# Performance work log

Measured on AMD Instinct MI355X. Metric: run time of the kernel, lower is better.

Reference implementation:

```python
import jax, jax.numpy as jnp
import numpy as np

N_NODES = 100000
N_EDGES = 1600000
IN_DIM = 128
HID = 128
OUT_DIM = 64
NLP_DIM = 786  # 768 + 11 + 4 + 3
N_LAYERS = 3
N_USERS = 4096
BN_EPS = 1e-5


def setup_inputs() -> dict:
    key = jax.random.key(0)
    ks = jax.random.split(key, 24)
    inp = {
        "x": jax.random.normal(ks[0], (N_NODES, IN_DIM), jnp.float32),
        "nlp_features": jax.random.normal(ks[1], (NLP_DIM,), jnp.float32),
        "edge_index": jax.random.randint(ks[2], (2, N_EDGES), 0, N_NODES),
        "user_indices": jax.random.randint(ks[3], (N_USERS,), 0, N_NODES),
        # input projection
        "W_in": jax.random.normal(ks[4], (IN_DIM, HID), jnp.float32) / np.sqrt(IN_DIM),
        "b_in": jnp.zeros((HID,), jnp.float32),
        # GCN layers (stacked)
        "W_gnn": jax.random.normal(ks[5], (N_LAYERS, HID, HID), jnp.float32) / np.sqrt(HID),
        "b_gnn": jnp.zeros((N_LAYERS, HID), jnp.float32),
        # batchnorm running stats / affine (eval mode)
        "bn_gamma": jnp.ones((N_LAYERS, HID), jnp.float32),
        "bn_beta": jnp.zeros((N_LAYERS, HID), jnp.float32),
        "bn_mean": 0.1 * jax.random.normal(ks[6], (N_LAYERS, HID), jnp.float32),
        "bn_var": 0.5 + jax.random.uniform(ks[7], (N_LAYERS, HID), jnp.float32),
        # node embedding projection
        "W_proj": jax.random.normal(ks[8], (HID, OUT_DIM), jnp.float32) / np.sqrt(HID),
        "b_proj": jnp.zeros((OUT_DIM,), jnp.float32),
        # predictor MLP
        "W1": jax.random.normal(ks[9], (OUT_DIM + NLP_DIM, 256), jnp.float32) / np.sqrt(OUT_DIM + NLP_DIM),
        "b1": jnp.zeros((256,), jnp.float32),
        "W2": jax.random.normal(ks[10], (256, 128), jnp.float32) / np.sqrt(256.0),
        "b2": jnp.zeros((128,), jnp.float32),
        "W3": jax.random.normal(ks[11], (128, 1), jnp.float32) / np.sqrt(128.0),
        "b3": jnp.zeros((1,), jnp.float32),
    }
    return inp


def reference(x, nlp_features, edge_index, user_indices,
              W_in, b_in, W_gnn, b_gnn, bn_gamma, bn_beta, bn_mean, bn_var,
              W_proj, b_proj, W1, b1, W2, b2, W3, b3):
    n = x.shape[0]
    src, dst = edge_index[0], edge_index[1]
    # GCN normalization with self-loops: deg = in-degree + 1
    deg = jax.ops.segment_sum(jnp.ones_like(src, dtype=x.dtype), dst, num_segments=n) + 1.0
    dinv = jax.lax.rsqrt(deg)                      # [N]
    enorm = dinv[src] * dinv[dst]                  # [E]

    h = jax.nn.relu(x @ W_in + b_in)               # [N, HID]
    for i in range(W_gnn.shape[0]):
        hw = h @ W_gnn[i]                          # [N, HID]
        agg = jax.ops.segment_sum(enorm[:, None] * hw[src], dst, num_segments=n)
        agg = agg + (dinv * dinv)[:, None] * hw + b_gnn[i]  # self-loop + bias
        # batchnorm (eval: running stats) + relu; dropout is identity in eval
        hn = (agg - bn_mean[i]) * jax.lax.rsqrt(bn_var[i] + BN_EPS) * bn_gamma[i] + bn_beta[i]
        h = jax.nn.relu(hn)

    emb = h @ W_proj + b_proj                      # [N, OUT_DIM]
    u = emb[user_indices]                          # [B, OUT_DIM]
    nlp = jnp.broadcast_to(nlp_features, (u.shape[0], nlp_features.shape[0]))
    z = jnp.concatenate([u, nlp], axis=1)          # [B, OUT_DIM+NLP_DIM]
    z = jax.nn.relu(z @ W1 + b1)
    z = jax.nn.relu(z @ W2 + b2)
    probs = jax.nn.sigmoid(z @ W3 + b3)
    return probs.squeeze(-1)
```

## Files before the change

kernel.cpp:

```cpp
#include <hip/hip_runtime.h>
#include <math.h>

typedef _Float16 half4 __attribute__((ext_vector_type(4)));


__global__ __launch_bounds__(256) void hist_k(const int* __restrict__ dst, int* __restrict__ cnt,
                                              int* __restrict__ rank, int E){
  int e = blockIdx.x*256 + threadIdx.x;
  if (e < E) rank[e] = atomicAdd(&cnt[dst[e]], 1);
}

__global__ __launch_bounds__(256) void blocksum_k(const int* __restrict__ cnt, int* __restrict__ bsum, int N){
  int i = blockIdx.x*256 + threadIdx.x;
  int v = (i < N) ? cnt[i] : 0;
  #pragma unroll
  for (int off = 32; off; off >>= 1) v += __shfl_down(v, off, 64);
  __shared__ int s[4];
  if ((threadIdx.x & 63) == 0) s[threadIdx.x >> 6] = v;
  __syncthreads();
  if (threadIdx.x == 0) bsum[blockIdx.x] = s[0] + s[1] + s[2] + s[3];
}

__global__ __launch_bounds__(512) void scan_small_k(const int* __restrict__ bsum, int* __restrict__ boff, int NB){
  __shared__ int s[512];
  int t = threadIdx.x;
  int v = (t < NB) ? bsum[t] : 0;
  s[t] = v; __syncthreads();
  for (int off = 1; off < 512; off <<= 1){
    int x = (t >= off) ? s[t-off] : 0;
    __syncthreads();
    s[t] += x;
    __syncthreads();
  }
  if (t < NB) boff[t] = s[t] - v;
}

__global__ __launch_bounds__(256) void scan_final_k(const int* __restrict__ cnt, const int* __restrict__ boff,
                                                    int* __restrict__ rowptr,
                                                    float* __restrict__ dinv, int N){
  __shared__ int s[256];
  int t = threadIdx.x;
  int i = blockIdx.x*256 + t;
  int v = (i < N) ? cnt[i] : 0;
  s[t] = v; __syncthreads();
  for (int off = 1; off < 256; off <<= 1){
    int x = (t >= off) ? s[t-off] : 0;
    __syncthreads();
    s[t] += x;
    __syncthreads();
  }
  int excl = s[t] - v + boff[blockIdx.x];
  if (i < N){
    rowptr[i] = excl;
    dinv[i]   = rsqrtf((float)v + 1.0f);
    if (i == N-1) rowptr[N] = excl + v;
  }
}

__global__ __launch_bounds__(256) void fill_k(const int* __restrict__ src, const int* __restrict__ dst,
                                              const int* __restrict__ rowptr, const int* __restrict__ rank,
                                              int* __restrict__ col, int E){
  int e = blockIdx.x*256 + threadIdx.x;
  if (e >= E) return;
  col[rowptr[dst[e]] + rank[e]] = src[e];
}


template<int ACT, int SCALED>
__global__ __launch_bounds__(256) void gemm128_k(const float* __restrict__ A, const float* __restrict__ B,
                                                 const float* __restrict__ bias, float* __restrict__ Cf,
                                                 _Float16* __restrict__ Ch, const float* __restrict__ dinv,
                                                 int M, int N, int K){
  __shared__ float As[16][132];
  __shared__ float Bs[16][132];
  const int tid = threadIdx.x;
  const int m0 = blockIdx.x * 128, n0 = blockIdx.y * 128;
  const int ty = tid >> 4, tx = tid & 15;
  const int sar = tid >> 1, sak = (tid & 1) * 8;
  const int sbk = tid >> 4, sbn = (tid & 15) * 8;
  int arow = m0 + sar; if (arow >= M) arow = M - 1;

  float acc[8][8];
  #pragma unroll
  for (int i = 0; i < 8; ++i)
    #pragma unroll
    for (int j = 0; j < 8; ++j) acc[i][j] = 0.f;

  float4 a0 = *(const float4*)&A[(size_t)arow*K + 0 + sak];
  float4 a1 = *(const float4*)&A[(size_t)arow*K + 0 + sak + 4];
  float4 b0 = *(const float4*)&B[(size_t)(0+sbk)*N + n0 + sbn];
  float4 b1 = *(const float4*)&B[(size_t)(0+sbk)*N + n0 + sbn + 4];

  for (int k0 = 0; k0 < K; k0 += 16){
    __syncthreads();
    As[sak+0][sar]=a0.x; As[sak+1][sar]=a0.y; As[sak+2][sar]=a0.z; As[sak+3][sar]=a0.w;
    As[sak+4][sar]=a1.x; As[sak+5][sar]=a1.y; As[sak+6][sar]=a1.z; As[sak+7][sar]=a1.w;
    *(float4*)&Bs[sbk][sbn]   = b0;
    *(float4*)&Bs[sbk][sbn+4] = b1;
    __syncthreads();
    if (k0 + 16 < K){
      a0 = *(const float4*)&A[(size_t)arow*K + (k0+16) + sak];
      a1 = *(const float4*)&A[(size_t)arow*K + (k0+16) + sak + 4];
      b0 = *(const float4*)&B[(size_t)(k0+16+sbk)*N + n0 + sbn];
      b1 = *(const float4*)&B[(size_t)(k0+16+sbk)*N + n0 + sbn + 4];
    }
    #pragma unroll
    for (int kk = 0; kk < 16; ++kk){
      const float4 av0 = *(const float4*)&As[kk][ty*4];
      const float4 av1 = *(const float4*)&As[kk][64 + ty*4];
      const float4 bv0 = *(const float4*)&Bs[kk][tx*4];
      const float4 bv1 = *(const float4*)&Bs[kk][64 + tx*4];
      const float a[8] = {av0.x,av0.y,av0.z,av0.w,av1.x,av1.y,av1.z,av1.w};
      const float b[8] = {bv0.x,bv0.y,bv0.z,bv0.w,bv1.x,bv1.y,bv1.z,bv1.w};
      #pragma unroll
      for (int i = 0; i < 8; ++i)
        #pragma unroll
        for (int j = 0; j < 8; ++j)
          acc[i][j] += a[i]*b[j];
    }
  }

  float bl[8] = {0,0,0,0,0,0,0,0};
  if (!SCALED && bias){
    const float4 x0 = *(const float4*)&bias[n0 + tx*4];
    const float4 x1 = *(const float4*)&bias[n0 + 64 + tx*4];
    bl[0]=x0.x; bl[1]=x0.y; bl[2]=x0.z; bl[3]=x0.w;
    bl[4]=x1.x; bl[5]=x1.y; bl[6]=x1.z; bl[7]=x1.w;
  }
  #pragma unroll
  for (int i = 0; i < 8; ++i){
    int r = m0 + (i>>2)*64 + ty*4 + (i&3);
    if (r < M){
      if (SCALED){
        float di = dinv[r];
        half4 h0, h1;
        h0[0]=(_Float16)(di*acc[i][0]); h0[1]=(_Float16)(di*acc[i][1]);
        h0[2]=(_Float16)(di*acc[i][2]); h0[3]=(_Float16)(di*acc[i][3]);
        h1[0]=(_Float16)(di*acc[i][4]); h1[1]=(_Float16)(di*acc[i][5]);
        h1[2]=(_Float16)(di*acc[i][6]); h1[3]=(_Float16)(di*acc[i][7]);
        *(half4*)&Ch[(size_t)r*N + n0 + tx*4]      = h0;
        *(half4*)&Ch[(size_t)r*N + n0 + 64 + tx*4] = h1;
      } else {
        float4 o0, o1;
        o0.x = acc[i][0]+bl[0]; o0.y = acc[i][1]+bl[1]; o0.z = acc[i][2]+bl[2]; o0.w = acc[i][3]+bl[3];
        o1.x = acc[i][4]+bl[4]; o1.y = acc[i][5]+bl[5]; o1.z = acc[i][6]+bl[6]; o1.w = acc[i][7]+bl[7];
        if (ACT == 1){
          o0.x=fmaxf(o0.x,0.f); o0.y=fmaxf(o0.y,0.f); o0.z=fmaxf(o0.z,0.f); o0.w=fmaxf(o0.w,0.f);
          o1.x=fmaxf(o1.x,0.f); o1.y=fmaxf(o1.y,0.f); o1.z=fmaxf(o1.z,0.f); o1.w=fmaxf(o1.w,0.f);
        }
        *(float4*)&Cf[(size_t)r*N + n0 + tx*4]      = o0;
        *(float4*)&Cf[(size_t)r*N + n0 + 64 + tx*4] = o1;
      }
    }
  }
}


template<int ACT>
__global__ __launch_bounds__(256) void gemm_k(const float* __restrict__ A, const float* __restrict__ B,
                                              const float* __restrict__ bias, float* __restrict__ C,
                                              int M, int N, int K){
  __shared__ float As[16][68];
  __shared__ float Bs[16][68];
  int tid = threadIdx.x;
  int m0 = blockIdx.x * 64, n0 = blockIdx.y * 64;
  int ty = tid >> 4, tx = tid & 15;
  int lm = tid >> 2, lkq = tid & 3;
  int lk = tid >> 4, ln4 = tid & 15;
  int arow = m0 + lm; if (arow >= M) arow = M - 1;

  float acc[4][4] = {{0.f}};

  for (int k0 = 0; k0 < K; k0 += 16){
    float4 av = *(const float4*)&A[(size_t)arow*K + k0 + lkq*4];
    float4 bv = *(const float4*)&B[(size_t)(k0+lk)*N + n0 + ln4*4];
    As[lkq*4+0][lm] = av.x; As[lkq*4+1][lm] = av.y; As[lkq*4+2][lm] = av.z; As[lkq*4+3][lm] = av.w;
    *(float4*)&Bs[lk][ln4*4] = bv;
    __syncthreads();
    #pragma unroll
    for (int kk = 0; kk < 16; ++kk){
      const float4 a = *(const float4*)&As[kk][ty*4];
      const float4 b = *(const float4*)&Bs[kk][tx*4];
      acc[0][0] += a.x*b.x; acc[0][1] += a.x*b.y; acc[0][2] += a.x*b.z; acc[0][3] += a.x*b.w;
      acc[1][0] += a.y*b.x; acc[1][1] += a.y*b.y; acc[1][2] += a.y*b.z; acc[1][3] += a.y*b.w;
      acc[2][0] += a.z*b.x; acc[2][1] += a.z*b.y; acc[2][2] += a.z*b.z; acc[2][3] += a.z*b.w;
      acc[3][0] += a.w*b.x; acc[3][1] += a.w*b.y; acc[3][2] += a.w*b.z; acc[3][3] += a.w*b.w;
    }
    __syncthreads();
  }

  float bv0 = 0.f, bv1 = 0.f, bv2 = 0.f, bv3 = 0.f;
  if (bias){
    const float4 b4 = *(const float4*)&bias[n0 + tx*4];
    bv0 = b4.x; bv1 = b4.y; bv2 = b4.z; bv3 = b4.w;
  }
  #pragma unroll
  for (int i = 0; i < 4; ++i){
    int r = m0 + ty*4 + i;
    if (r < M){
      float4 o;
      o.x = acc[i][0] + bv0; o.y = acc[i][1] + bv1; o.z = acc[i][2] + bv2; o.w = acc[i][3] + bv3;
      if (ACT == 1){ o.x = fmaxf(o.x,0.f); o.y = fmaxf(o.y,0.f); o.z = fmaxf(o.z,0.f); o.w = fmaxf(o.w,0.f); }
      *(float4*)&C[(size_t)r*N + n0 + tx*4] = o;
    }
  }
}


__global__ __launch_bounds__(256) void agg_k(const _Float16* __restrict__ hws, float* __restrict__ hout,
                                             const int* __restrict__ rowptr, const int* __restrict__ col,
                                             const float* __restrict__ dinv,
                                             const float* __restrict__ bgnn, const float* __restrict__ gamma,
                                             const float* __restrict__ beta, const float* __restrict__ mean,
                                             const float* __restrict__ var, int N){
  int n = (blockIdx.x * blockDim.x + threadIdx.x) >> 6;
  if (n >= N) return;
  int lane = threadIdx.x & 63;
  int half = lane >> 5;
  int sl   = lane & 31;
  int f    = sl * 4;
  int beg = rowptr[n], end = rowptr[n+1];

  float4 A0 = make_float4(0.f,0.f,0.f,0.f);
  float4 A1 = make_float4(0.f,0.f,0.f,0.f);
  float4 A2 = make_float4(0.f,0.f,0.f,0.f);
  float4 A3 = make_float4(0.f,0.f,0.f,0.f);

  int j = beg + half;
  for (; j + 6 < end; j += 8){
    int s0 = col[j], s1 = col[j+2], s2 = col[j+4], s3 = col[j+6];
    const half4 v0 = *(const half4*)&hws[(size_t)s0*128 + f];
    const half4 v1 = *(const half4*)&hws[(size_t)s1*128 + f];
    const half4 v2 = *(const half4*)&hws[(size_t)s2*128 + f];
    const half4 v3 = *(const half4*)&hws[(size_t)s3*128 + f];
    A0.x += (float)v0[0]; A0.y += (float)v0[1]; A0.z += (float)v0[2]; A0.w += (float)v0[3];
    A1.x += (float)v1[0]; A1.y += (float)v1[1]; A1.z += (float)v1[2]; A1.w += (float)v1[3];
    A2.x += (float)v2[0]; A2.y += (float)v2[1]; A2.z += (float)v2[2]; A2.w += (float)v2[3];
    A3.x += (float)v3[0]; A3.y += (float)v3[1]; A3.z += (float)v3[2]; A3.w += (float)v3[3];
  }
  for (; j < end; j += 2){
    int s0 = col[j];
    const half4 v0 = *(const half4*)&hws[(size_t)s0*128 + f];
    A0.x += (float)v0[0]; A0.y += (float)v0[1]; A0.z += (float)v0[2]; A0.w += (float)v0[3];
  }
  A0.x += A1.x + A2.x + A3.x;
  A0.y += A1.y + A2.y + A3.y;
  A0.z += A1.z + A2.z + A3.z;
  A0.w += A1.w + A2.w + A3.w;

  A0.x += __shfl_xor(A0.x, 32, 64);
  A0.y += __shfl_xor(A0.y, 32, 64);
  A0.z += __shfl_xor(A0.z, 32, 64);
  A0.w += __shfl_xor(A0.w, 32, 64);

  if (half == 0){
    float di = dinv[n];
    const half4 hv = *(const half4*)&hws[(size_t)n*128 + f];
    const float4 bg = *(const float4*)&bgnn[f];
    const float4 gm = *(const float4*)&gamma[f];
    const float4 bt = *(const float4*)&beta[f];
    const float4 mn = *(const float4*)&mean[f];
    const float4 vr = *(const float4*)&var[f];
    float4 o;
    o.x = (di*(A0.x + (float)hv[0]) + bg.x - mn.x) * (gm.x * rsqrtf(vr.x + 1e-5f)) + bt.x;
    o.y = (di*(A0.y + (float)hv[1]) + bg.y - mn.y) * (gm.y * rsqrtf(vr.y + 1e-5f)) + bt.y;
    o.z = (di*(A0.z + (float)hv[2]) + bg.z - mn.z) * (gm.z * rsqrtf(vr.z + 1e-5f)) + bt.z;
    o.w = (di*(A0.w + (float)hv[3]) + bg.w - mn.w) * (gm.w * rsqrtf(vr.w + 1e-5f)) + bt.w;
    o.x = fmaxf(o.x, 0.f); o.y = fmaxf(o.y, 0.f); o.z = fmaxf(o.z, 0.f); o.w = fmaxf(o.w, 0.f);
    *(float4*)&hout[(size_t)n*128 + f] = o;
  }
}


__global__ __launch_bounds__(256) void gather_k(const float* __restrict__ h, const int* __restrict__ uidx,
                                                float* __restrict__ uh, int B){
  int g = blockIdx.x*256 + threadIdx.x;
  if (g >= B*128) return;
  int i = g >> 7, f = g & 127;
  uh[g] = h[(size_t)uidx[i]*128 + f];
}

__global__ __launch_bounds__(256) void initc1_k(const float* __restrict__ b1, float* __restrict__ c1){
  c1[threadIdx.x] = b1[threadIdx.x];
}

__global__ __launch_bounds__(256) void c1acc_k(const float* __restrict__ nlp, const float* __restrict__ W1,
                                               float* __restrict__ c1, int NLP){
  int b = blockIdx.x;
  int c  = (b & 3) * 64 + (threadIdx.x & 63);
  int dq = threadIdx.x >> 6;
  int d0 = (b >> 2) * 99;
  float acc = 0.f;
  for (int d = d0 + dq; d < d0 + 99 && d < NLP; d += 4)
    acc += nlp[d] * W1[(size_t)(64 + d) * 256 + c];
  __shared__ float s[256];
  s[threadIdx.x] = acc; __syncthreads();
  if (dq == 0){
    float t = s[threadIdx.x] + s[threadIdx.x + 64] + s[threadIdx.x + 128] + s[threadIdx.x + 192];
    atomicAdd(&c1[c], t);
  }
}

__global__ __launch_bounds__(256) void head_k(const float* __restrict__ z2, const float* __restrict__ W3,
                                              const float* __restrict__ b3, float* __restrict__ out, int B){
  int gid = blockIdx.x * blockDim.x + threadIdx.x;
  int u = gid >> 6, l = gid & 63;
  if (u >= B) return;
  float v = z2[(size_t)u*128 + l] * W3[l] + z2[(size_t)u*128 + 64 + l] * W3[64 + l];
  #pragma unroll
  for (int off = 32; off; off >>= 1) v += __shfl_down(v, off, 64);
  if (l == 0) out[u] = 1.f / (1.f + expf(-(v + b3[0])));
}


static void launch_gemm(int act, const float* A, const float* Bm, const float* bias, float* C,
                        int M, int N, int K, hipStream_t s){
  dim3 g((M + 63) / 64, N / 64);
  if (act) hipLaunchKernelGGL((gemm_k<1>), g, dim3(256), 0, s, A, Bm, bias, C, M, N, K);
  else     hipLaunchKernelGGL((gemm_k<0>), g, dim3(256), 0, s, A, Bm, bias, C, M, N, K);
}

extern "C" void kernel_launch(void* const* d_in, const int* in_sizes, int n_in,
                              void* d_out, int out_size, void* d_ws, size_t ws_size,
                              hipStream_t stream){
  const float* x     = (const float*)d_in[0];
  const float* nlp   = (const float*)d_in[1];
  const int*   eidx  = (const int*)  d_in[2];
  const int*   uidx  = (const int*)  d_in[3];
  const float* W_in  = (const float*)d_in[4];
  const float* b_in  = (const float*)d_in[5];
  const float* W_gnn = (const float*)d_in[6];
  const float* b_gnn = (const float*)d_in[7];
  const float* gam   = (const float*)d_in[8];
  const float* bet   = (const float*)d_in[9];
  const float* mean  = (const float*)d_in[10];
  const float* var   = (const float*)d_in[11];
  const float* Wproj = (const float*)d_in[12];
  const float* bproj = (const float*)d_in[13];
  const float* W1    = (const float*)d_in[14];
  const float* b1    = (const float*)d_in[15];
  const float* W2    = (const float*)d_in[16];
  const float* b2    = (const float*)d_in[17];
  const float* W3    = (const float*)d_in[18];
  const float* b3    = (const float*)d_in[19];
  float* out = (float*)d_out;

  const int N   = in_sizes[0] / 128;
  const int E   = in_sizes[2] / 2;
  const int B   = in_sizes[3];
  const int NLP = in_sizes[1];
  const int HID = 128;

  char* p = (char*)d_ws;
  auto carve = [&](size_t bytes) -> void* {
    void* q = (void*)p;
    p += (bytes + 255) & ~(size_t)255;
    return q;
  };
  int*      cnt    = (int*)     carve((size_t)N * 4);
  int*      rowptr = (int*)     carve((size_t)(N + 1) * 4);
  int*      rank   = (int*)     carve((size_t)E * 4);
  int*      bsum   = (int*)     carve(512 * 4);
  int*      boff   = (int*)     carve(512 * 4);
  float*    dinv   = (float*)   carve((size_t)N * 4);
  int*      col    = (int*)     carve((size_t)E * 4);
  float*    h      = (float*)   carve((size_t)N * HID * 4);
  _Float16* hws    = (_Float16*)carve((size_t)N * HID * 2);
  float*    uh     = (float*)   carve((size_t)B * HID * 4);
  float*    embu   = (float*)   carve((size_t)B * 64 * 4);
  float*    z1     = (float*)   carve((size_t)B * 256 * 4);
  float*    z2     = (float*)   carve((size_t)B * 128 * 4);
  float*    c1     = (float*)   carve(256 * 4);

  const int* src = eidx;
  const int* dst = eidx + E;

  const int NB = (N + 255) / 256;

  hipMemsetAsync(cnt, 0, (size_t)N * 4, stream);
  hipLaunchKernelGGL(hist_k, dim3((E + 255) / 256), dim3(256), 0, stream, dst, cnt, rank, E);
  hipLaunchKernelGGL(blocksum_k, dim3(NB), dim3(256), 0, stream, cnt, bsum, N);
  hipLaunchKernelGGL(scan_small_k, dim3(1), dim3(512), 0, stream, bsum, boff, NB);
  hipLaunchKernelGGL(scan_final_k, dim3(NB), dim3(256), 0, stream, cnt, boff, rowptr, dinv, N);
  hipLaunchKernelGGL(fill_k, dim3((E + 255) / 256), dim3(256), 0, stream, src, dst, rowptr, rank, col, E);

  {
    dim3 g((N + 127) / 128, HID / 128);
    hipLaunchKernelGGL((gemm128_k<1,0>), g, dim3(256), 0, stream,
                       x, W_in, b_in, h, (_Float16*)nullptr, (const float*)nullptr, N, HID, 128);
  }

  for (int i = 0; i < 3; ++i){
    dim3 g((N + 127) / 128, HID / 128);
    hipLaunchKernelGGL((gemm128_k<0,1>), g, dim3(256), 0, stream,
                       h, W_gnn + (size_t)i * 128 * 128, (const float*)nullptr,
                       (float*)nullptr, hws, dinv, N, HID, 128);
    hipLaunchKernelGGL(agg_k, dim3((N * 64 + 255) / 256), dim3(256), 0, stream,
                       hws, h, rowptr, col, dinv,
                       b_gnn + i * 128, gam + i * 128, bet + i * 128, mean + i * 128, var + i * 128, N);
  }

  hipLaunchKernelGGL(gather_k, dim3((B * 128 + 255) / 256), dim3(256), 0, stream, h, uidx, uh, B);
  hipLaunchKernelGGL(initc1_k, dim3(1), dim3(256), 0, stream, b1, c1);
  hipLaunchKernelGGL(c1acc_k, dim3(32), dim3(256), 0, stream, nlp, W1, c1, NLP);

  launch_gemm(0, uh, Wproj, bproj, embu, B, 64, 128, stream);
  launch_gemm(1, embu, W1, c1, z1, B, 256, 64, stream);
  launch_gemm(1, z1, W2, b2, z2, B, 128, 256, stream);
  hipLaunchKernelGGL(head_k, dim3((B * 64 + 255) / 256), dim3(256), 0, stream, z2, W3, b3, out, B);
}
```

Before: 698.1 us.

## Use MFMA fp16 GEMMs with swizzled LDS and store hidden state in fp16

Replaces the fp32 SIMT 128x128 GEMM with an MFMA 16x16x32 fp16 kernel. Weights are pre-transposed and converted to fp16, and both operands are staged in LDS with an XOR swizzle. The hidden state h is now stored in fp16, which halves GEMM input and aggregation output traffic, and the aggregation accumulates neighbours in fp16 half4 vectors instead of fp32. This lowers memory and compute cost but risks precision loss from fp16 accumulation over neighbour sums. The 64KB of LDS per block may also limit occupancy.

```diff
diff --git a/kernel.cpp b/kernel.cpp
--- a/kernel.cpp
+++ b/kernel.cpp
@@ -1,7 +1,9 @@
 #include <hip/hip_runtime.h>
 #include <math.h>
 
-typedef _Float16 half4 __attribute__((ext_vector_type(4)));
+typedef _Float16 half8_t __attribute__((ext_vector_type(8)));
+typedef _Float16 half4_t __attribute__((ext_vector_type(4)));
+typedef float    f32x4_t __attribute__((ext_vector_type(4)));
 
 
 __global__ __launch_bounds__(256) void hist_k(const int* __restrict__ dst, int* __restrict__ cnt,
@@ -66,90 +68,116 @@
 }
 
 
-template<int ACT, int SCALED>
-__global__ __launch_bounds__(256) void gemm128_k(const float* __restrict__ A, const float* __restrict__ B,
-                                                 const float* __restrict__ bias, float* __restrict__ Cf,
-                                                 _Float16* __restrict__ Ch, const float* __restrict__ dinv,
-                                                 int M, int N, int K){
-  __shared__ float As[16][132];
-  __shared__ float Bs[16][132];
+__global__ __launch_bounds__(256) void prepw_k(const float* __restrict__ Win, const float* __restrict__ Wgnn,
+                                               _Float16* __restrict__ Bt){
+  int idx = blockIdx.x*256 + threadIdx.x;
+  int m = idx >> 14;
+  int r = idx & 16383;
+  int k = r >> 7, n = r & 127;
+  const float* W = (m == 0) ? Win : (Wgnn + (size_t)(m-1)*16384);
+  Bt[(size_t)m*16384 + n*128 + k] = (_Float16)W[k*128 + n];
+}
+
+
+template<int AF16, int EPI>
+__global__ __launch_bounds__(256) void mgemm_k(const void* __restrict__ Ap, const _Float16* __restrict__ Bt,
+                                               const float* __restrict__ bias, const float* __restrict__ dinv,
+                                               _Float16* __restrict__ C, int M){
+  __shared__ _Float16 As[128*128];
+  __shared__ _Float16 Bs[128*128];
   const int tid = threadIdx.x;
-  const int m0 = blockIdx.x * 128, n0 = blockIdx.y * 128;
-  const int ty = tid >> 4, tx = tid & 15;
-  const int sar = tid >> 1, sak = (tid & 1) * 8;
-  const int sbk = tid >> 4, sbn = (tid & 15) * 8;
-  int arow = m0 + sar; if (arow >= M) arow = M - 1;
-
-  float acc[8][8];
-  #pragma unroll
-  for (int i = 0; i < 8; ++i)
-    #pragma unroll
-    for (int j = 0; j < 8; ++j) acc[i][j] = 0.f;
-
-  float4 a0 = *(const float4*)&A[(size_t)arow*K + 0 + sak];
-  float4 a1 = *(const float4*)&A[(size_t)arow*K + 0 + sak + 4];
-  float4 b0 = *(const float4*)&B[(size_t)(0+sbk)*N + n0 + sbn];
-  float4 b1 = *(const float4*)&B[(size_t)(0+sbk)*N + n0 + sbn + 4];
-
-  for (int k0 = 0; k0 < K; k0 += 16){
-    __syncthreads();
-    As[sak+0][sar]=a0.x; As[sak+1][sar]=a0.y; As[sak+2][sar]=a0.z; As[sak+3][sar]=a0.w;
-    As[sak+4][sar]=a1.x; As[sak+5][sar]=a1.y; As[sak+6][sar]=a1.z; As[sak+7][sar]=a1.w;
-    *(float4*)&Bs[sbk][sbn]   = b0;
-    *(float4*)&Bs[sbk][sbn+4] = b1;
-    __syncthreads();
-    if (k0 + 16 < K){
-      a0 = *(const float4*)&A[(size_t)arow*K + (k0+16) + sak];
-      a1 = *(const float4*)&A[(size_t)arow*K + (k0+16) + sak + 4];
-      b0 = *(const float4*)&B[(size_t)(k0+16+sbk)*N + n0 + sbn];
-      b1 = *(const float4*)&B[(size_t)(k0+16+sbk)*N + n0 + sbn + 4];
-    }
-    #pragma unroll
-    for (int kk = 0; kk < 16; ++kk){
-      const float4 av0 = *(const float4*)&As[kk][ty*4];
-      const float4 av1 = *(const float4*)&As[kk][64 + ty*4];
-      const float4 bv0 = *(const float4*)&Bs[kk][tx*4];
-      const float4 bv1 = *(const float4*)&Bs[kk][64 + tx*4];
-      const float a[8] = {av0.x,av0.y,av0.z,av0.w,av1.x,av1.y,av1.z,av1.w};
-      const float b[8] = {bv0.x,bv0.y,bv0.z,bv0.w,bv1.x,bv1.y,bv1.z,bv1.w};
+  const int m0 = blockIdx.x * 128;
+
+  {
+    int n = tid >> 1, kb = (tid & 1) * 64;
+    const half8_t* srcb = (const half8_t*)(Bt + n*128 + kb);
+    #pragma unroll
+    for (int q = 0; q < 8; ++q){
+      uint32_t byte = (uint32_t)(n*256 + kb*2 + q*16) ^ (uint32_t)((n & 7) << 4);
+      *(half8_t*)((char*)Bs + byte) = srcb[q];
+    }
+  }
+  {
+    int rr = tid >> 1, kb = (tid & 1) * 64;
+    int row = m0 + rr; if (row >= M) row = M - 1;
+    if (AF16){
+      const half8_t* srca = (const half8_t*)((const _Float16*)Ap + (size_t)row*128 + kb);
       #pragma unroll
-      for (int i = 0; i < 8; ++i)
-        #pragma unroll
-        for (int j = 0; j < 8; ++j)
-          acc[i][j] += a[i]*b[j];
-    }
-  }
-
-  float bl[8] = {0,0,0,0,0,0,0,0};
-  if (!SCALED && bias){
-    const float4 x0 = *(const float4*)&bias[n0 + tx*4];
-    const float4 x1 = *(const float4*)&bias[n0 + 64 + tx*4];
-    bl[0]=x0.x; bl[1]=x0.y; bl[2]=x0.z; bl[3]=x0.w;
-    bl[4]=x1.x; bl[5]=x1.y; bl[6]=x1.z; bl[7]=x1.w;
-  }
-  #pragma unroll
-  for (int i = 0; i < 8; ++i){
-    int r = m0 + (i>>2)*64 + ty*4 + (i&3);
-    if (r < M){
-      if (SCALED){
-        float di = dinv[r];
-        half4 h0, h1;
-        h0[0]=(_Float16)(di*acc[i][0]); h0[1]=(_Float16)(di*acc[i][1]);
-        h0[2]=(_Float16)(di*acc[i][2]); h0[3]=(_Float16)(di*acc[i][3]);
-        h1[0]=(_Float16)(di*acc[i][4]); h1[1]=(_Float16)(di*acc[i][5]);
-        h1[2]=(_Float16)(di*acc[i][6]); h1[3]=(_Float16)(di*acc[i][7]);
-        *(half4*)&Ch[(size_t)r*N + n0 + tx*4]      = h0;
-        *(half4*)&Ch[(size_t)r*N + n0 + 64 + tx*4] = h1;
-      } else {
-        float4 o0, o1;
-        o0.x = acc[i][0]+bl[0]; o0.y = acc[i][1]+bl[1]; o0.z = acc[i][2]+bl[2]; o0.w = acc[i][3]+bl[3];
-        o1.x = acc[i][4]+bl[4]; o1.y = acc[i][5]+bl[5]; o1.z = acc[i][6]+bl[6]; o1.w = acc[i][7]+bl[7];
-        if (ACT == 1){
-          o0.x=fmaxf(o0.x,0.f); o0.y=fmaxf(o0.y,0.f); o0.z=fmaxf(o0.z,0.f); o0.w=fmaxf(o0.w,0.f);
-          o1.x=fmaxf(o1.x,0.f); o1.y=fmaxf(o1.y,0.f); o1.z=fmaxf(o1.z,0.f); o1.w=fmaxf(o1.w,0.f);
+      for (int q = 0; q < 8; ++q){
+        uint32_t byte = (uint32_t)(rr*256 + kb*2 + q*16) ^ (uint32_t)((rr & 7) << 4);
+        *(half8_t*)((char*)As + byte) = srca[q];
+      }
+    } else {
+      const float4* srca = (const float4*)((const float*)Ap + (size_t)row*128 + kb);
+      #pragma unroll
+      for (int q = 0; q < 8; ++q){
+        float4 f0 = srca[2*q], f1 = srca[2*q+1];
+        half8_t h;
+        h[0]=(_Float16)f0.x; h[1]=(_Float16)f0.y; h[2]=(_Float16)f0.z; h[3]=(_Float16)f0.w;
+        h[4]=(_Float16)f1.x; h[5]=(_Float16)f1.y; h[6]=(_Float16)f1.z; h[7]=(_Float16)f1.w;
+        uint32_t byte = (uint32_t)(rr*256 + kb*2 + q*16) ^ (uint32_t)((rr & 7) << 4);
+        *(half8_t*)((char*)As + byte) = h;
+      }
+    }
+  }
+  __syncthreads();
+
+  const int w = tid >> 6, lane = tid & 63;
+  const int l15 = lane & 15, lq = lane >> 4;
+
+  f32x4_t acc[2][8];
+  #pragma unroll
+  for (int rg = 0; rg < 2; ++rg)
+    #pragma unroll
+    for (int cg = 0; cg < 8; ++cg)
+      acc[rg][cg] = (f32x4_t){0.f,0.f,0.f,0.f};
+
+  #pragma unroll
+  for (int ks = 0; ks < 4; ++ks){
+    half8_t a[2], b[8];
+    #pragma unroll
+    for (int rg = 0; rg < 2; ++rg){
+      int row = w*32 + rg*16 + l15;
+      uint32_t byte = (uint32_t)(row*256 + (ks*32 + lq*8)*2) ^ (uint32_t)((row & 7) << 4);
+      a[rg] = *(const half8_t*)((const char*)As + byte);
+    }
+    #pragma unroll
+    for (int cg = 0; cg < 8; ++cg){
+      int coln = cg*16 + l15;
+      uint32_t byte = (uint32_t)(coln*256 + (ks*32 + lq*8)*2) ^ (uint32_t)((coln & 7) << 4);
+      b[cg] = *(const half8_t*)((const char*)Bs + byte);
+    }
+    #pragma unroll
+    for (int rg = 0; rg < 2; ++rg)
+      #pragma unroll
+      for (int cg = 0; cg < 8; ++cg)
+        acc[rg][cg] = __builtin_amdgcn_mfma_f32_16x16x32_f16(a[rg], b[cg], acc[rg][cg], 0, 0, 0);
+  }
+
+  float bl[8];
+  if (EPI == 0){
+    #pragma unroll
+    for (int cg = 0; cg < 8; ++cg) bl[cg] = bias[cg*16 + l15];
+  }
+
+  #pragma unroll
+  for (int rg = 0; rg < 2; ++rg){
+    #pragma unroll
+    for (int r = 0; r < 4; ++r){
+      int grow = m0 + w*32 + rg*16 + lq*4 + r;
+      if (grow < M){
+        if (EPI == 1){
+          float di = dinv[grow];
+          #pragma unroll
+          for (int cg = 0; cg < 8; ++cg)
+            C[(size_t)grow*128 + cg*16 + l15] = (_Float16)(di * acc[rg][cg][r]);
+        } else {
+          #pragma unroll
+          for (int cg = 0; cg < 8; ++cg){
+            float v = acc[rg][cg][r] + bl[cg];
+            C[(size_t)grow*128 + cg*16 + l15] = (_Float16)fmaxf(v, 0.f);
+          }
         }
-        *(float4*)&Cf[(size_t)r*N + n0 + tx*4]      = o0;
-        *(float4*)&Cf[(size_t)r*N + n0 + 64 + tx*4] = o1;
       }
     }
   }
@@ -207,7 +235,7 @@
 }
 
 
-__global__ __launch_bounds__(256) void agg_k(const _Float16* __restrict__ hws, float* __restrict__ hout,
+__global__ __launch_bounds__(256) void agg_k(const _Float16* __restrict__ hws, _Float16* __restrict__ hout,
                                              const int* __restrict__ rowptr, const int* __restrict__ col,
                                              const float* __restrict__ dinv,
                                              const float* __restrict__ bgnn, const float* __restrict__ gamma,
@@ -221,32 +249,26 @@
   int f    = sl * 4;
   int beg = rowptr[n], end = rowptr[n+1];
 
-  float4 A0 = make_float4(0.f,0.f,0.f,0.f);
-  float4 A1 = make_float4(0.f,0.f,0.f,0.f);
-  float4 A2 = make_float4(0.f,0.f,0.f,0.f);
-  float4 A3 = make_float4(0.f,0.f,0.f,0.f);
+  half4_t H0 = {0,0,0,0}, H1 = {0,0,0,0}, H2 = {0,0,0,0}, H3 = {0,0,0,0};
 
   int j = beg + half;
   for (; j + 6 < end; j += 8){
     int s0 = col[j], s1 = col[j+2], s2 = col[j+4], s3 = col[j+6];
-    const half4 v0 = *(const half4*)&hws[(size_t)s0*128 + f];
-    const half4 v1 = *(const half4*)&hws[(size_t)s1*128 + f];
-    const half4 v2 = *(const half4*)&hws[(size_t)s2*128 + f];
-    const half4 v3 = *(const half4*)&hws[(size_t)s3*128 + f];
-    A0.x += (float)v0[0]; A0.y += (float)v0[1]; A0.z += (float)v0[2]; A0.w += (float)v0[3];
-    A1.x += (float)v1[0]; A1.y += (float)v1[1]; A1.z += (float)v1[2]; A1.w += (float)v1[3];
-    A2.x += (float)v2[0]; A2.y += (float)v2[1]; A2.z += (float)v2[2]; A2.w += (float)v2[3];
-    A3.x += (float)v3[0]; A3.y += (float)v3[1]; A3.z += (float)v3[2]; A3.w += (float)v3[3];
+    H0 += *(const half4_t*)&hws[(size_t)s0*128 + f];
+    H1 += *(const half4_t*)&hws[(size_t)s1*128 + f];
+    H2 += *(const half4_t*)&hws[(size_t)s2*128 + f];
+    H3 += *(const half4_t*)&hws[(size_t)s3*128 + f];
   }
   for (; j < end; j += 2){
     int s0 = col[j];
-    const half4 v0 = *(const half4*)&hws[(size_t)s0*128 + f];
-    A0.x += (float)v0[0]; A0.y += (float)v0[1]; A0.z += (float)v0[2]; A0.w += (float)v0[3];
-  }
-  A0.x += A1.x + A2.x + A3.x;
-  A0.y += A1.y + A2.y + A3.y;
-  A0.z += A1.z + A2.z + A3.z;
-  A0.w += A1.w + A2.w + A3.w;
+    H0 += *(const half4_t*)&hws[(size_t)s0*128 + f];
+  }
+
+  float4 A0;
+  A0.x = (float)H0[0] + (float)H1[0] + (float)H2[0] + (float)H3[0];
+  A0.y = (float)H0[1] + (float)H1[1] + (float)H2[1] + (float)H3[1];
+  A0.z = (float)H0[2] + (float)H1[2] + (float)H2[2] + (float)H3[2];
+  A0.w = (float)H0[3] + (float)H1[3] + (float)H2[3] + (float)H3[3];
 
   A0.x += __shfl_xor(A0.x, 32, 64);
   A0.y += __shfl_xor(A0.y, 32, 64);
@@ -255,29 +277,32 @@
 
   if (half == 0){
     float di = dinv[n];
-    const half4 hv = *(const half4*)&hws[(size_t)n*128 + f];
+    const half4_t hv = *(const half4_t*)&hws[(size_t)n*128 + f];
     const float4 bg = *(const float4*)&bgnn[f];
     const float4 gm = *(const float4*)&gamma[f];
     const float4 bt = *(const float4*)&beta[f];
     const float4 mn = *(const float4*)&mean[f];
     const float4 vr = *(const float4*)&var[f];
-    float4 o;
-    o.x = (di*(A0.x + (float)hv[0]) + bg.x - mn.x) * (gm.x * rsqrtf(vr.x + 1e-5f)) + bt.x;
-    o.y = (di*(A0.y + (float)hv[1]) + bg.y - mn.y) * (gm.y * rsqrtf(vr.y + 1e-5f)) + bt.y;
-    o.z = (di*(A0.z + (float)hv[2]) + bg.z - mn.z) * (gm.z * rsqrtf(vr.z + 1e-5f)) + bt.z;
-    o.w = (di*(A0.w + (float)hv[3]) + bg.w - mn.w) * (gm.w * rsqrtf(vr.w + 1e-5f)) + bt.w;
-    o.x = fmaxf(o.x, 0.f); o.y = fmaxf(o.y, 0.f); o.z = fmaxf(o.z, 0.f); o.w = fmaxf(o.w, 0.f);
-    *(float4*)&hout[(size_t)n*128 + f] = o;
-  }
-}
-
-
-__global__ __launch_bounds__(256) void gather_k(const float* __restrict__ h, const int* __restrict__ uidx,
+    float o0 = (di*(A0.x + (float)hv[0]) + bg.x - mn.x) * (gm.x * rsqrtf(vr.x + 1e-5f)) + bt.x;
+    float o1 = (di*(A0.y + (float)hv[1]) + bg.y - mn.y) * (gm.y * rsqrtf(vr.y + 1e-5f)) + bt.y;
+    float o2 = (di*(A0.z + (float)hv[2]) + bg.z - mn.z) * (gm.z * rsqrtf(vr.z + 1e-5f)) + bt.z;
+    float o3 = (di*(A0.w + (float)hv[3]) + bg.w - mn.w) * (gm.w * rsqrtf(vr.w + 1e-5f)) + bt.w;
+    half4_t o;
+    o[0] = (_Float16)fmaxf(o0, 0.f);
+    o[1] = (_Float16)fmaxf(o1, 0.f);
+    o[2] = (_Float16)fmaxf(o2, 0.f);
+    o[3] = (_Float16)fmaxf(o3, 0.f);
+    *(half4_t*)&hout[(size_t)n*128 + f] = o;
+  }
+}
+
+
+__global__ __launch_bounds__(256) void gather_k(const _Float16* __restrict__ h, const int* __restrict__ uidx,
                                                 float* __restrict__ uh, int B){
   int g = blockIdx.x*256 + threadIdx.x;
   if (g >= B*128) return;
   int i = g >> 7, f = g & 127;
-  uh[g] = h[(size_t)uidx[i]*128 + f];
+  uh[g] = (float)h[(size_t)uidx[i]*128 + f];
 }
 
 __global__ __launch_bounds__(256) void initc1_k(const float* __restrict__ b1, float* __restrict__ c1){
@@ -364,7 +389,8 @@
   int*      boff   = (int*)     carve(512 * 4);
   float*    dinv   = (float*)   carve((size_t)N * 4);
   int*      col    = (int*)     carve((size_t)E * 4);
-  float*    h      = (float*)   carve((size_t)N * HID * 4);
+  _Float16* Bt     = (_Float16*)carve((size_t)4 * 128 * 128 * 2);
+  _Float16* h      = (_Float16*)carve((size_t)N * HID * 2);
   _Float16* hws    = (_Float16*)carve((size_t)N * HID * 2);
   float*    uh     = (float*)   carve((size_t)B * HID * 4);
   float*    embu   = (float*)   carve((size_t)B * 64 * 4);
@@ -376,6 +402,7 @@
   const int* dst = eidx + E;
 
   const int NB = (N + 255) / 256;
+  const int GB = (N + 127) / 128;
 
   hipMemsetAsync(cnt, 0, (size_t)N * 4, stream);
   hipLaunchKernelGGL(hist_k, dim3((E + 255) / 256), dim3(256), 0, stream, dst, cnt, rank, E);
@@ -384,17 +411,14 @@
   hipLaunchKernelGGL(scan_final_k, dim3(NB), dim3(256), 0, stream, cnt, boff, rowptr, dinv, N);
   hipLaunchKernelGGL(fill_k, dim3((E + 255) / 256), dim3(256), 0, stream, src, dst, rowptr, rank, col, E);
 
-  {
-    dim3 g((N + 127) / 128, HID / 128);
-    hipLaunchKernelGGL((gemm128_k<1,0>), g, dim3(256), 0, stream,
-                       x, W_in, b_in, h, (_Float16*)nullptr, (const float*)nullptr, N, HID, 128);
-  }
+  hipLaunchKernelGGL(prepw_k, dim3(256), dim3(256), 0, stream, W_in, W_gnn, Bt);
+
+  hipLaunchKernelGGL((mgemm_k<0,0>), dim3(GB), dim3(256), 0, stream,
+                     (const void*)x, Bt, b_in, (const float*)nullptr, h, N);
 
   for (int i = 0; i < 3; ++i){
-    dim3 g((N + 127) / 128, HID / 128);
-    hipLaunchKernelGGL((gemm128_k<0,1>), g, dim3(256), 0, stream,
-                       h, W_gnn + (size_t)i * 128 * 128, (const float*)nullptr,
-                       (float*)nullptr, hws, dinv, N, HID, 128);
+    hipLaunchKernelGGL((mgemm_k<1,1>), dim3(GB), dim3(256), 0, stream,
+                       (const void*)h, Bt + (size_t)(i+1)*16384, (const float*)nullptr, dinv, hws, N);
     hipLaunchKernelGGL(agg_k, dim3((N * 64 + 255) / 256), dim3(256), 0, stream,
                        hws, h, rowptr, col, dinv,
                        b_gnn + i * 128, gam + i * 128, bet + i * 128, mean + i * 128, var + i * 128, N);
```

After: 567.5 us. -18.7%, faster.
